# Optimization experiments

Measured on AMD Instinct MI355X. Metric: run time of the kernel, lower is better.

The kernel has to match this reference:

```python
import jax, jax.numpy as jnp
import numpy as np

N_NODES = 50000
N_EDGES = 600000
D = 128
BN_EPS = 1e-5


def _linear_init(key, fan_in, fan_out):
    # torch nn.Linear default: U(-1/sqrt(fan_in), 1/sqrt(fan_in)) for W and b
    kw, kb = jax.random.split(key)
    bound = 1.0 / np.sqrt(fan_in)
    W = jax.random.uniform(kw, (fan_in, fan_out), minval=-bound, maxval=bound, dtype=jnp.float32)
    b = jax.random.uniform(kb, (fan_out,), minval=-bound, maxval=bound, dtype=jnp.float32)
    return W, b


def setup_inputs() -> dict:
    key = jax.random.key(0)
    ks = jax.random.split(key, 8)
    x = jax.random.normal(ks[0], (N_NODES, D), dtype=jnp.float32)
    edge_index = jax.random.randint(ks[1], (2, N_EDGES), 0, N_NODES, dtype=jnp.int32)
    edge_attr = jax.random.normal(ks[2], (N_EDGES, D), dtype=jnp.float32)
    # MLP: [2D, D, D, D] -> Linear(2D,D)+SiLU+BN, Linear(D,D)+SiLU+BN, Linear(D,D)
    W1, b1 = _linear_init(ks[3], 2 * D, D)
    W2, b2 = _linear_init(ks[4], D, D)
    W3, b3 = _linear_init(ks[5], D, D)
    g1 = jnp.ones((D,), jnp.float32); be1 = jnp.zeros((D,), jnp.float32)
    g2 = jnp.ones((D,), jnp.float32); be2 = jnp.zeros((D,), jnp.float32)
    return {"x": x, "edge_index": edge_index, "edge_attr": edge_attr,
            "W1": W1, "b1": b1, "g1": g1, "be1": be1,
            "W2": W2, "b2": b2, "g2": g2, "be2": be2,
            "W3": W3, "b3": b3}


def _bn(h, gamma, beta):
    # BatchNorm1d in training mode: normalize with batch statistics (biased var)
    mean = jnp.mean(h, axis=0)
    var = jnp.var(h, axis=0)
    return (h - mean) * jax.lax.rsqrt(var + BN_EPS) * gamma + beta


def reference(x, edge_index, edge_attr, W1, b1, g1, be1, W2, b2, g2, be2, W3, b3):
    src = edge_index[0]
    # scatter_add over edges indexed by source node -> [N_NODES, D]
    agg = jax.ops.segment_sum(edge_attr, src, num_segments=x.shape[0])
    h = jnp.concatenate([x, agg], axis=1)  # [N, 2D]
    h = _bn(jax.nn.silu(h @ W1 + b1), g1, be1)
    h = _bn(jax.nn.silu(h @ W2 + b2), g2, be2)
    return h @ W3 + b3
```

## Files before the change

kernel.cpp:

```cpp
#include <hip/hip_runtime.h>
#include <hip/hip_bf16.h>

#define D 128

typedef __attribute__((ext_vector_type(8))) short bfrag;
typedef __attribute__((ext_vector_type(4))) float facc;
typedef __attribute__((ext_vector_type(4))) unsigned int u32x4;
typedef __attribute__((ext_vector_type(4))) float f32x4;

__device__ __forceinline__ facc mfma16(bfrag a, bfrag b, facc c) {
    return __builtin_amdgcn_mfma_f32_16x16x32_bf16(a, b, c, 0, 0, 0);
}
__device__ __forceinline__ unsigned int bf16_rn(float f) {
    unsigned int u = __float_as_uint(f);
    u += 0x7FFF + ((u >> 16) & 1);
    return u >> 16;
}
__device__ __forceinline__ float bf16_f(unsigned int h) {
    return __uint_as_float(h << 16);
}
__device__ __forceinline__ unsigned int packf(float v) {
    unsigned int hi = bf16_rn(v);
    unsigned int lo = bf16_rn(v - bf16_f(hi));
    return (hi << 16) | lo;
}

__global__ __launch_bounds__(256) void prep_kernel(
    const int* __restrict__ src, int* __restrict__ counts, int nedges,
    const float* __restrict__ x, unsigned int* __restrict__ xp, int n4,
    const float* __restrict__ W1, unsigned short* __restrict__ Wh,
    unsigned short* __restrict__ Wl, int eblk, int sblk) {
    int b = blockIdx.x;
    if (b < eblk) {
        int e = b * 256 + threadIdx.x;
        if (e < nedges) atomicAdd(&counts[src[e]], 1);
    } else if (b < eblk + sblk) {
        int i = (b - eblk) * 256 + threadIdx.x;
        if (i < n4) {
            float4 v = ((const float4*)x)[i];
            uint4 p;
            p.x = packf(v.x);
            p.y = packf(v.y);
            p.z = packf(v.z);
            p.w = packf(v.w);
            ((uint4*)xp)[i] = p;
        }
    } else {
        int j = b - eblk - sblk;
        int k = threadIdx.x;
        float w = W1[(size_t)k * D + j];
        unsigned int hi = bf16_rn(w);
        size_t o = (size_t)((k >> 3) * 128 + j) * 8 + (k & 7);
        Wh[o] = (unsigned short)hi;
        Wl[o] = (unsigned short)bf16_rn(w - bf16_f(hi));
    }
}

#define SCHUNK 2048
__global__ __launch_bounds__(256) void scan1_kernel(
    const int* __restrict__ counts, int* __restrict__ bsum, int n) {
    __shared__ int sd[256];
    const int tid = threadIdx.x;
    const int base = blockIdx.x * SCHUNK + tid * 8;
    int s = 0;
#pragma unroll
    for (int j = 0; j < 8; ++j) {
        int idx = base + j;
        if (idx < n) s += counts[idx];
    }
    sd[tid] = s;
    __syncthreads();
    for (int d2 = 128; d2; d2 >>= 1) {
        if (tid < d2) sd[tid] += sd[tid + d2];
        __syncthreads();
    }
    if (tid == 0) bsum[blockIdx.x] = sd[0];
}
__global__ void scan2_kernel(int* __restrict__ bsum, int nb) {
    int tid = threadIdx.x;
    int v = (tid < nb) ? bsum[tid] : 0;
#pragma unroll
    for (int d2 = 1; d2 < 64; d2 <<= 1) {
        int t = __shfl_up(v, d2);
        if (tid >= d2) v += t;
    }
    if (tid < nb) bsum[tid] = v;
}
__global__ __launch_bounds__(256) void scan3_kernel(
    const int* __restrict__ counts, const int* __restrict__ bsum,
    int* __restrict__ off, int* __restrict__ cur, int n) {
    __shared__ int sd[256];
    const int tid = threadIdx.x;
    const int base = blockIdx.x * SCHUNK + tid * 8;
    int loc[8];
    int s = 0;
#pragma unroll
    for (int j = 0; j < 8; ++j) {
        int idx = base + j;
        int c = (idx < n) ? counts[idx] : 0;
        loc[j] = c;
        s += c;
    }
    sd[tid] = s;
    __syncthreads();
#pragma unroll
    for (int d2 = 1; d2 < 256; d2 <<= 1) {
        int t = (tid >= d2) ? sd[tid - d2] : 0;
        __syncthreads();
        sd[tid] += t;
        __syncthreads();
    }
    int boff = (blockIdx.x == 0) ? 0 : bsum[blockIdx.x - 1];
    int pre = boff + sd[tid] - s;
#pragma unroll
    for (int j = 0; j < 8; ++j) {
        int idx = base + j;
        if (idx < n) {
            off[idx] = pre;
            cur[idx] = pre;
            pre += loc[j];
        }
    }
    if (tid == 255 && base + 8 >= n && n <= blockIdx.x * SCHUNK + SCHUNK)
        off[n] = boff + sd[255];
}

__global__ void fill_kernel(const int* __restrict__ src, int* __restrict__ cur,
                            int* __restrict__ eid, int nedges) {
    int e = blockIdx.x * 256 + threadIdx.x;
    if (e < nedges) {
        int slot = atomicAdd(&cur[src[e]], 1);
        eid[slot] = e;
    }
}

__global__ __launch_bounds__(256) void gather_kernel(
    const float* __restrict__ edge_attr, const int* __restrict__ eid,
    const int* __restrict__ off, unsigned int* __restrict__ aggp, int nnodes) {
    int node = blockIdx.x * 4 + (threadIdx.x >> 6);
    int lane = threadIdx.x & 63;
    if (node >= nnodes) return;
    const int h = lane >> 5;
    const int c = lane & 31;
    int i = off[node];
    const int e = off[node + 1];
    f32x4 acc = {0.f, 0.f, 0.f, 0.f};

    if (i < e && (i & 1)) {
        f32x4 v = __builtin_nontemporal_load(
            (const f32x4*)(edge_attr + (size_t)eid[i] * D) + c);
        if (h == 0) acc += v;
        ++i;
    }
    for (; i + 16 <= e; i += 16) {
        f32x4 v[8];
#pragma unroll
        for (int u = 0; u < 8; ++u) {
            int2 ep = *(const int2*)(eid + i + 2 * u);
            int row = h ? ep.y : ep.x;
            v[u] = __builtin_nontemporal_load(
                (const f32x4*)(edge_attr + (size_t)row * D) + c);
        }
#pragma unroll
        for (int u = 0; u < 8; ++u) acc += v[u];
    }
    for (; i + 2 <= e; i += 2) {
        int2 ep = *(const int2*)(eid + i);
        int row = h ? ep.y : ep.x;
        acc += __builtin_nontemporal_load(
            (const f32x4*)(edge_attr + (size_t)row * D) + c);
    }
    if (i < e) {
        f32x4 v = __builtin_nontemporal_load(
            (const f32x4*)(edge_attr + (size_t)eid[i] * D) + c);
        if (h == 0) acc += v;
    }
#pragma unroll
    for (int r = 0; r < 4; ++r) acc[r] += __shfl_xor(acc[r], 32);
    if (h == 0) {
        u32x4 p;
#pragma unroll
        for (int r = 0; r < 4; ++r) p[r] = packf(acc[r]);
        *((u32x4*)(aggp + (size_t)node * D) + c) = p;
    }
}

__global__ void fold_kernel(const float* __restrict__ sum,
                            const float* __restrict__ sq,
                            const float* __restrict__ gamma,
                            const float* __restrict__ beta,
                            const float* __restrict__ W,
                            const float* __restrict__ b,
                            unsigned short* __restrict__ Wh,
                            unsigned short* __restrict__ Wl,
                            float* __restrict__ bf, float invM) {
    int j = blockIdx.x;
    int k = threadIdx.x;
    float mean = sum[k] * invM;
    float var = sq[k] * invM - mean * mean;
    float scale = gamma[k] * rsqrtf(var + 1e-5f);
    float shift = beta[k] - mean * scale;
    float w = W[k * D + j];
    float wf = scale * w;
    unsigned int hi = bf16_rn(wf);
    size_t o = (size_t)((k >> 3) * 128 + j) * 8 + (k & 7);
    Wh[o] = (unsigned short)hi;
    Wl[o] = (unsigned short)bf16_rn(wf - bf16_f(hi));
    float v = shift * w;
#pragma unroll
    for (int of = 32; of; of >>= 1) v += __shfl_down(v, of);
    __shared__ float ws2[2];
    if ((k & 63) == 0) ws2[k >> 6] = v;
    __syncthreads();
    if (k == 0) bf[j] = b[j] + ws2[0] + ws2[1];
}

template <int K, bool SILU, bool STATS, bool PACKOUT>
__global__ __launch_bounds__(256, 2) void gemm_mfma(
    const unsigned int* __restrict__ A0, const unsigned int* __restrict__ A1,
    const unsigned short* __restrict__ Wh,
    const unsigned short* __restrict__ Wl,
    const float* __restrict__ bias, unsigned int* __restrict__ Cp,
    float* __restrict__ Cf, float* __restrict__ gsum,
    float* __restrict__ gsq, int M) {
    constexpr int NS = K / 32;
    const int tid = threadIdx.x;
    const int w = tid >> 6;
    const int l = tid & 63;
    const int lr = l & 15;
    const int lk = l >> 4;
    const int row0 = blockIdx.x * 128 + w * 32;

    facc acc[2][8];
#pragma unroll
    for (int rt = 0; rt < 2; ++rt)
#pragma unroll
        for (int ct = 0; ct < 8; ++ct)
#pragma unroll
            for (int r = 0; r < 4; ++r) acc[rt][ct][r] = 0.f;

    for (int s = 0; s < NS; ++s) {
        const int kb = s * 32 + lk * 8;
        bfrag ah[2], al[2];
#pragma unroll
        for (int rt = 0; rt < 2; ++rt) {
            const int arow = row0 + rt * 16 + lr;
            const unsigned int* As = A0;
            int kk = kb;
            if (K == 256 && s >= 4) { As = A1; kk = kb - 128; }
            u32x4 q0 = {0u, 0u, 0u, 0u}, q1 = {0u, 0u, 0u, 0u};
            if (arow < M) {
                const u32x4* p = (const u32x4*)(As + (size_t)arow * D + kk);
                q0 = p[0];
                q1 = p[1];
            }
            unsigned int ua[8] = {q0.x, q0.y, q0.z, q0.w,
                                  q1.x, q1.y, q1.z, q1.w};
            u32x4 uh, ul;
#pragma unroll
            for (int r = 0; r < 4; ++r) {
                uh[r] = __builtin_amdgcn_perm(ua[2 * r + 1], ua[2 * r],
                                              0x07060302u);
                ul[r] = __builtin_amdgcn_perm(ua[2 * r + 1], ua[2 * r],
                                              0x05040100u);
            }
            ah[rt] = __builtin_bit_cast(bfrag, uh);
            al[rt] = __builtin_bit_cast(bfrag, ul);
        }
        bfrag bh[8], bl[8];
        const int fb = (s * 4 + lk) * 128;
#pragma unroll
        for (int ct = 0; ct < 8; ++ct) {
            size_t o = (size_t)(fb + ct * 16 + lr) * 8;
            bh[ct] = *(const bfrag*)(Wh + o);
            bl[ct] = *(const bfrag*)(Wl + o);
        }
#pragma unroll
        for (int rt = 0; rt < 2; ++rt)
#pragma unroll
            for (int ct = 0; ct < 8; ++ct)
                acc[rt][ct] = mfma16(ah[rt], bh[ct], acc[rt][ct]);
#pragma unroll
        for (int rt = 0; rt < 2; ++rt)
#pragma unroll
            for (int ct = 0; ct < 8; ++ct)
                acc[rt][ct] = mfma16(ah[rt], bl[ct], acc[rt][ct]);
#pragma unroll
        for (int rt = 0; rt < 2; ++rt)
#pragma unroll
            for (int ct = 0; ct < 8; ++ct)
                acc[rt][ct] = mfma16(al[rt], bh[ct], acc[rt][ct]);
    }

    __shared__ float sred[2][4][128];
#pragma unroll
    for (int ct = 0; ct < 8; ++ct) {
        const int col = ct * 16 + lr;
        const float bj = bias[col];
        float s = 0.f, q = 0.f;
#pragma unroll
        for (int rt = 0; rt < 2; ++rt) {
            const int base = row0 + rt * 16 + lk * 4;
#pragma unroll
            for (int r = 0; r < 4; ++r) {
                int crow = base + r;
                if (crow < M) {
                    float v = acc[rt][ct][r] + bj;
                    if (SILU) v = v / (1.0f + __expf(-v));
                    if (PACKOUT) Cp[(size_t)crow * D + col] = packf(v);
                    else         Cf[(size_t)crow * D + col] = v;
                    if (STATS) { s += v; q += v * v; }
                }
            }
        }
        if (STATS) {
            s += __shfl_xor(s, 16);
            s += __shfl_xor(s, 32);
            q += __shfl_xor(q, 16);
            q += __shfl_xor(q, 32);
            if (lk == 0) {
                sred[0][w][col] = s;
                sred[1][w][col] = q;
            }
        }
    }
    if (STATS) {
        __syncthreads();
        if (tid < 128) {
            float v = sred[0][0][tid] + sred[0][1][tid] + sred[0][2][tid] +
                      sred[0][3][tid];
            unsafeAtomicAdd(&gsum[tid], v);
        } else {
            int c = tid - 128;
            float v = sred[1][0][c] + sred[1][1][c] + sred[1][2][c] +
                      sred[1][3][c];
            unsafeAtomicAdd(&gsq[c], v);
        }
    }
}

extern "C" void kernel_launch(void* const* d_in, const int* in_sizes, int n_in,
                              void* d_out, int out_size, void* d_ws,
                              size_t ws_size, hipStream_t stream) {
    const float* x     = (const float*)d_in[0];
    const int*   eidx  = (const int*)d_in[1];
    const float* eattr = (const float*)d_in[2];
    const float* W1  = (const float*)d_in[3];
    const float* b1  = (const float*)d_in[4];
    const float* g1  = (const float*)d_in[5];
    const float* be1 = (const float*)d_in[6];
    const float* W2  = (const float*)d_in[7];
    const float* b2  = (const float*)d_in[8];
    const float* g2  = (const float*)d_in[9];
    const float* be2 = (const float*)d_in[10];
    const float* W3  = (const float*)d_in[11];
    const float* b3  = (const float*)d_in[12];

    const int M = in_sizes[0] / D;
    const int E = in_sizes[1] / 2;
    const int* srcIdx = eidx;

    unsigned int* wsu = (unsigned int*)d_ws;
    unsigned int* aggp = wsu;
    unsigned int* xp   = aggp + (size_t)M * D;
    unsigned int* h1p  = xp + (size_t)M * D;
    unsigned int* h2p  = h1p + (size_t)M * D;
    float* sum1 = (float*)(h2p + (size_t)M * D);
    float* sq1  = sum1 + D;
    float* sum2 = sq1 + D;
    float* sq2  = sum2 + D;
    float* b2f  = sq2 + D;
    float* b3f  = b2f + D;
    int* counts = (int*)(b3f + D);
    int* off    = counts + M;
    int* cur    = off + M + 4;
    int* eid    = cur + M;
    int* bsum   = eid + E;
    unsigned short* W1h = (unsigned short*)(bsum + 64);
    unsigned short* W1l = W1h + 256 * D;
    unsigned short* W2h = W1l + 256 * D;
    unsigned short* W2l = W2h + D * D;
    unsigned short* W3h = W2l + D * D;
    unsigned short* W3l = W3h + D * D;

    float* out = (float*)d_out;

    hipMemsetAsync(counts, 0, (size_t)M * sizeof(int), stream);
    hipMemsetAsync(sum1, 0, 4 * D * sizeof(float), stream);

    const int eblk = (E + 255) / 256;
    const int sblk = (M * 32 + 255) / 256;
    prep_kernel<<<eblk + sblk + 128, 256, 0, stream>>>(
        srcIdx, counts, E, x, xp, M * 32, W1, W1h, W1l, eblk, sblk);

    const int nb = (M + SCHUNK - 1) / SCHUNK;
    scan1_kernel<<<nb, 256, 0, stream>>>(counts, bsum, M);
    scan2_kernel<<<1, 64, 0, stream>>>(bsum, nb);
    scan3_kernel<<<nb, 256, 0, stream>>>(counts, bsum, off, cur, M);
    fill_kernel<<<eblk, 256, 0, stream>>>(srcIdx, cur, eid, E);
    gather_kernel<<<(M + 3) / 4, 256, 0, stream>>>(eattr, eid, off, aggp, M);

    int nblk = (M + 127) / 128;
    gemm_mfma<256, true, true, true><<<nblk, 256, 0, stream>>>(
        xp, aggp, W1h, W1l, b1, h1p, nullptr, sum1, sq1, M);
    fold_kernel<<<D, D, 0, stream>>>(sum1, sq1, g1, be1, W2, b2, W2h, W2l,
                                     b2f, 1.0f / (float)M);
    gemm_mfma<128, true, true, true><<<nblk, 256, 0, stream>>>(
        h1p, nullptr, W2h, W2l, b2f, h2p, nullptr, sum2, sq2, M);
    fold_kernel<<<D, D, 0, stream>>>(sum2, sq2, g2, be2, W3, b3, W3h, W3l,
                                     b3f, 1.0f / (float)M);
    gemm_mfma<128, false, false, false><<<nblk, 256, 0, stream>>>(
        h2p, nullptr, W3h, W3l, b3f, nullptr, out, nullptr, nullptr, M);
}
```

Measured before the change: 247.7 us.

## Scatter bf16 edge rows into CSR order and fuse aggregation into first GEMM

Instead of building an edge-id permutation and gathering fp32 edge rows at random, the fill pass now reads each edge row once, converts it to bf16 and writes it into its CSR slot. The first GEMM then sums the contiguous, sorted rows per node into shared memory and consumes them directly as the second half of K. This removes the separate gather kernel, the eid indirection and the aggregated fp32 round trip. It trades a bf16 rounding of edge attributes, which lowers accuracy of the sums, and a 64-row tile GEMM with serial per-node aggregation.

```diff
diff --git a/kernel.cpp b/kernel.cpp
--- a/kernel.cpp
+++ b/kernel.cpp
@@ -6,6 +6,7 @@
 typedef __attribute__((ext_vector_type(8))) short bfrag;
 typedef __attribute__((ext_vector_type(4))) float facc;
 typedef __attribute__((ext_vector_type(4))) unsigned int u32x4;
+typedef __attribute__((ext_vector_type(2))) unsigned int u32x2;
 typedef __attribute__((ext_vector_type(4))) float f32x4;
 
 __device__ __forceinline__ facc mfma16(bfrag a, bfrag b, facc c) {
@@ -23,6 +24,12 @@
     unsigned int hi = bf16_rn(v);
     unsigned int lo = bf16_rn(v - bf16_f(hi));
     return (hi << 16) | lo;
+}
+__device__ __forceinline__ float bf16lo(unsigned int u) {
+    return __uint_as_float(u << 16);
+}
+__device__ __forceinline__ float bf16hi(unsigned int u) {
+    return __uint_as_float(u & 0xFFFF0000u);
 }
 
 __global__ __launch_bounds__(256) void prep_kernel(
@@ -125,63 +132,185 @@
         off[n] = boff + sd[255];
 }
 
-__global__ void fill_kernel(const int* __restrict__ src, int* __restrict__ cur,
-                            int* __restrict__ eid, int nedges) {
-    int e = blockIdx.x * 256 + threadIdx.x;
-    if (e < nedges) {
-        int slot = atomicAdd(&cur[src[e]], 1);
-        eid[slot] = e;
-    }
-}
-
-__global__ __launch_bounds__(256) void gather_kernel(
-    const float* __restrict__ edge_attr, const int* __restrict__ eid,
-    const int* __restrict__ off, unsigned int* __restrict__ aggp, int nnodes) {
-    int node = blockIdx.x * 4 + (threadIdx.x >> 6);
-    int lane = threadIdx.x & 63;
-    if (node >= nnodes) return;
-    const int h = lane >> 5;
-    const int c = lane & 31;
-    int i = off[node];
-    const int e = off[node + 1];
-    f32x4 acc = {0.f, 0.f, 0.f, 0.f};
-
-    if (i < e && (i & 1)) {
-        f32x4 v = __builtin_nontemporal_load(
-            (const f32x4*)(edge_attr + (size_t)eid[i] * D) + c);
-        if (h == 0) acc += v;
-        ++i;
-    }
-    for (; i + 16 <= e; i += 16) {
-        f32x4 v[8];
-#pragma unroll
-        for (int u = 0; u < 8; ++u) {
-            int2 ep = *(const int2*)(eid + i + 2 * u);
-            int row = h ? ep.y : ep.x;
-            v[u] = __builtin_nontemporal_load(
-                (const f32x4*)(edge_attr + (size_t)row * D) + c);
-        }
-#pragma unroll
-        for (int u = 0; u < 8; ++u) acc += v[u];
-    }
-    for (; i + 2 <= e; i += 2) {
-        int2 ep = *(const int2*)(eid + i);
-        int row = h ? ep.y : ep.x;
-        acc += __builtin_nontemporal_load(
-            (const f32x4*)(edge_attr + (size_t)row * D) + c);
-    }
-    if (i < e) {
-        f32x4 v = __builtin_nontemporal_load(
-            (const f32x4*)(edge_attr + (size_t)eid[i] * D) + c);
-        if (h == 0) acc += v;
-    }
-#pragma unroll
-    for (int r = 0; r < 4; ++r) acc[r] += __shfl_xor(acc[r], 32);
-    if (h == 0) {
-        u32x4 p;
-#pragma unroll
-        for (int r = 0; r < 4; ++r) p[r] = packf(acc[r]);
-        *((u32x4*)(aggp + (size_t)node * D) + c) = p;
+__global__ __launch_bounds__(256) void fillp_kernel(
+    const float* __restrict__ edge_attr, const int* __restrict__ src,
+    int* __restrict__ cur, unsigned int* __restrict__ ebS, int nedges) {
+    const int l = threadIdx.x & 63;
+    const int h = l >> 5;
+    const int c = l & 31;
+    int e = blockIdx.x * 8 + (threadIdx.x >> 6) * 2 + h;
+    if (e >= nedges) return;
+    f32x4 v = __builtin_nontemporal_load(
+        (const f32x4*)(edge_attr + (size_t)e * D) + c);
+    int slot = 0;
+    if (c == 0) slot = atomicAdd(&cur[src[e]], 1);
+    slot = __shfl(slot, l & 32);
+    u32x2 p;
+    p.x = bf16_rn(v[0]) | (bf16_rn(v[1]) << 16);
+    p.y = bf16_rn(v[2]) | (bf16_rn(v[3]) << 16);
+    *((u32x2*)(ebS + (size_t)slot * 64) + c) = p;
+}
+
+__global__ __launch_bounds__(256, 2) void gemm1_fused(
+    const unsigned int* __restrict__ xp, const unsigned int* __restrict__ ebS,
+    const int* __restrict__ off, const unsigned short* __restrict__ Wh,
+    const unsigned short* __restrict__ Wl, const float* __restrict__ bias,
+    unsigned int* __restrict__ h1p, float* __restrict__ gsum,
+    float* __restrict__ gsq, int M) {
+    __shared__ unsigned int As[64][132];
+    __shared__ float sred[2][4][128];
+    const int tid = threadIdx.x;
+    const int w = tid >> 6;
+    const int l = tid & 63;
+    const int h = l >> 5;
+    const int c = l & 31;
+    const int row0 = blockIdx.x * 64;
+
+    for (int nd = 0; nd < 16; ++nd) {
+        int node = row0 + w * 16 + nd;
+        if (node >= M) break;
+        int s = off[node];
+        const int e = off[node + 1];
+        f32x4 acc = {0.f, 0.f, 0.f, 0.f};
+        int i = s;
+        for (; i + 16 <= e; i += 16) {
+            u32x2 q[8];
+#pragma unroll
+            for (int u = 0; u < 8; ++u)
+                q[u] = __builtin_nontemporal_load(
+                    (const u32x2*)(ebS + (size_t)(i + 2 * u + h) * 64) + c);
+#pragma unroll
+            for (int u = 0; u < 8; ++u) {
+                acc[0] += bf16lo(q[u].x);
+                acc[1] += bf16hi(q[u].x);
+                acc[2] += bf16lo(q[u].y);
+                acc[3] += bf16hi(q[u].y);
+            }
+        }
+        for (; i + 2 <= e; i += 2) {
+            u32x2 q = __builtin_nontemporal_load(
+                (const u32x2*)(ebS + (size_t)(i + h) * 64) + c);
+            acc[0] += bf16lo(q.x);
+            acc[1] += bf16hi(q.x);
+            acc[2] += bf16lo(q.y);
+            acc[3] += bf16hi(q.y);
+        }
+        if (i < e && h == 0) {
+            u32x2 q = __builtin_nontemporal_load(
+                (const u32x2*)(ebS + (size_t)i * 64) + c);
+            acc[0] += bf16lo(q.x);
+            acc[1] += bf16hi(q.x);
+            acc[2] += bf16lo(q.y);
+            acc[3] += bf16hi(q.y);
+        }
+#pragma unroll
+        for (int r = 0; r < 4; ++r) acc[r] += __shfl_xor(acc[r], 32);
+        if (h == 0) {
+            u32x4 p;
+#pragma unroll
+            for (int r = 0; r < 4; ++r) p[r] = packf(acc[r]);
+            *(u32x4*)&As[w * 16 + nd][c * 4] = p;
+        }
+    }
+    __syncthreads();
+
+    const int lr = l & 15;
+    const int lk = l >> 4;
+    facc acc[8];
+#pragma unroll
+    for (int ct = 0; ct < 8; ++ct)
+#pragma unroll
+        for (int r = 0; r < 4; ++r) acc[ct][r] = 0.f;
+
+    for (int s = 0; s < 8; ++s) {
+        unsigned int ua[8];
+        if (s < 4) {
+            const int arow = row0 + w * 16 + lr;
+            const int kk = s * 32 + lk * 8;
+            u32x4 q0 = {0u, 0u, 0u, 0u}, q1 = {0u, 0u, 0u, 0u};
+            if (arow < M) {
+                const u32x4* p = (const u32x4*)(xp + (size_t)arow * D + kk);
+                q0 = p[0];
+                q1 = p[1];
+            }
+#pragma unroll
+            for (int r = 0; r < 4; ++r) {
+                ua[r] = q0[r];
+                ua[4 + r] = q1[r];
+            }
+        } else {
+            const int kk = (s - 4) * 32 + lk * 8;
+            const u32x4* p = (const u32x4*)&As[w * 16 + lr][kk];
+            u32x4 q0 = p[0], q1 = p[1];
+#pragma unroll
+            for (int r = 0; r < 4; ++r) {
+                ua[r] = q0[r];
+                ua[4 + r] = q1[r];
+            }
+        }
+        u32x4 uh, ul;
+#pragma unroll
+        for (int r = 0; r < 4; ++r) {
+            uh[r] = __builtin_amdgcn_perm(ua[2 * r + 1], ua[2 * r],
+                                          0x07060302u);
+            ul[r] = __builtin_amdgcn_perm(ua[2 * r + 1], ua[2 * r],
+                                          0x05040100u);
+        }
+        bfrag ah = __builtin_bit_cast(bfrag, uh);
+        bfrag al = __builtin_bit_cast(bfrag, ul);
+
+        bfrag bh[8], bl[8];
+        const int fb = (s * 4 + lk) * 128;
+#pragma unroll
+        for (int ct = 0; ct < 8; ++ct) {
+            size_t o = (size_t)(fb + ct * 16 + lr) * 8;
+            bh[ct] = *(const bfrag*)(Wh + o);
+            bl[ct] = *(const bfrag*)(Wl + o);
+        }
+#pragma unroll
+        for (int ct = 0; ct < 8; ++ct) acc[ct] = mfma16(ah, bh[ct], acc[ct]);
+#pragma unroll
+        for (int ct = 0; ct < 8; ++ct) acc[ct] = mfma16(ah, bl[ct], acc[ct]);
+#pragma unroll
+        for (int ct = 0; ct < 8; ++ct) acc[ct] = mfma16(al, bh[ct], acc[ct]);
+    }
+
+#pragma unroll
+    for (int ct = 0; ct < 8; ++ct) {
+        const int col = ct * 16 + lr;
+        const float bj = bias[col];
+        float s = 0.f, q = 0.f;
+        const int base = row0 + w * 16 + lk * 4;
+#pragma unroll
+        for (int r = 0; r < 4; ++r) {
+            int crow = base + r;
+            if (crow < M) {
+                float v = acc[ct][r] + bj;
+                v = v / (1.0f + __expf(-v));
+                h1p[(size_t)crow * D + col] = packf(v);
+                s += v;
+                q += v * v;
+            }
+        }
+        s += __shfl_xor(s, 16);
+        s += __shfl_xor(s, 32);
+        q += __shfl_xor(q, 16);
+        q += __shfl_xor(q, 32);
+        if (lk == 0) {
+            sred[0][w][col] = s;
+            sred[1][w][col] = q;
+        }
+    }
+    __syncthreads();
+    if (tid < 128) {
+        float v = sred[0][0][tid] + sred[0][1][tid] + sred[0][2][tid] +
+                  sred[0][3][tid];
+        unsafeAtomicAdd(&gsum[tid], v);
+    } else {
+        int cc = tid - 128;
+        float v = sred[1][0][cc] + sred[1][1][cc] + sred[1][2][cc] +
+                  sred[1][3][cc];
+        unsafeAtomicAdd(&gsq[cc], v);
     }
 }
 
@@ -215,15 +344,14 @@
     if (k == 0) bf[j] = b[j] + ws2[0] + ws2[1];
 }
 
-template <int K, bool SILU, bool STATS, bool PACKOUT>
+template <bool SILU, bool STATS, bool PACKOUT>
 __global__ __launch_bounds__(256, 2) void gemm_mfma(
-    const unsigned int* __restrict__ A0, const unsigned int* __restrict__ A1,
+    const unsigned int* __restrict__ A0,
     const unsigned short* __restrict__ Wh,
     const unsigned short* __restrict__ Wl,
     const float* __restrict__ bias, unsigned int* __restrict__ Cp,
     float* __restrict__ Cf, float* __restrict__ gsum,
     float* __restrict__ gsq, int M) {
-    constexpr int NS = K / 32;
     const int tid = threadIdx.x;
     const int w = tid >> 6;
     const int l = tid & 63;
@@ -239,18 +367,15 @@
 #pragma unroll
             for (int r = 0; r < 4; ++r) acc[rt][ct][r] = 0.f;
 
-    for (int s = 0; s < NS; ++s) {
+    for (int s = 0; s < 4; ++s) {
         const int kb = s * 32 + lk * 8;
         bfrag ah[2], al[2];
 #pragma unroll
         for (int rt = 0; rt < 2; ++rt) {
             const int arow = row0 + rt * 16 + lr;
-            const unsigned int* As = A0;
-            int kk = kb;
-            if (K == 256 && s >= 4) { As = A1; kk = kb - 128; }
             u32x4 q0 = {0u, 0u, 0u, 0u}, q1 = {0u, 0u, 0u, 0u};
             if (arow < M) {
-                const u32x4* p = (const u32x4*)(As + (size_t)arow * D + kk);
+                const u32x4* p = (const u32x4*)(A0 + (size_t)arow * D + kb);
                 q0 = p[0];
                 q1 = p[1];
             }
@@ -361,10 +486,10 @@
     const int* srcIdx = eidx;
 
     unsigned int* wsu = (unsigned int*)d_ws;
-    unsigned int* aggp = wsu;
-    unsigned int* xp   = aggp + (size_t)M * D;
-    unsigned int* h1p  = xp + (size_t)M * D;
-    unsigned int* h2p  = h1p + (size_t)M * D;
+    unsigned int* ebS = wsu;
+    unsigned int* xp  = ebS + (size_t)E * 64;
+    unsigned int* h1p = xp + (size_t)M * D;
+    unsigned int* h2p = h1p + (size_t)M * D;
     float* sum1 = (float*)(h2p + (size_t)M * D);
     float* sq1  = sum1 + D;
     float* sum2 = sq1 + D;
@@ -374,8 +499,7 @@
     int* counts = (int*)(b3f + D);
     int* off    = counts + M;
     int* cur    = off + M + 4;
-    int* eid    = cur + M;
-    int* bsum   = eid + E;
+    int* bsum   = cur + M;
     unsigned short* W1h = (unsigned short*)(bsum + 64);
     unsigned short* W1l = W1h + 256 * D;
     unsigned short* W2h = W1l + 256 * D;
@@ -385,8 +509,8 @@
 
     float* out = (float*)d_out;
 
-    hipMemsetAsync(counts, 0, (size_t)M * sizeof(int), stream);
-    hipMemsetAsync(sum1, 0, 4 * D * sizeof(float), stream);
+    (void)hipMemsetAsync(counts, 0, (size_t)M * sizeof(int), stream);
+    (void)hipMemsetAsync(sum1, 0, 4 * D * sizeof(float), stream);
 
     const int eblk = (E + 255) / 256;
     const int sblk = (M * 32 + 255) / 256;
@@ -397,18 +521,19 @@
     scan1_kernel<<<nb, 256, 0, stream>>>(counts, bsum, M);
     scan2_kernel<<<1, 64, 0, stream>>>(bsum, nb);
     scan3_kernel<<<nb, 256, 0, stream>>>(counts, bsum, off, cur, M);
-    fill_kernel<<<eblk, 256, 0, stream>>>(srcIdx, cur, eid, E);
-    gather_kernel<<<(M + 3) / 4, 256, 0, stream>>>(eattr, eid, off, aggp, M);
+
+    fillp_kernel<<<(E + 7) / 8, 256, 0, stream>>>(eattr, srcIdx, cur, ebS, E);
+
+    gemm1_fused<<<(M + 63) / 64, 256, 0, stream>>>(
+        xp, ebS, off, W1h, W1l, b1, h1p, sum1, sq1, M);
 
     int nblk = (M + 127) / 128;
-    gemm_mfma<256, true, true, true><<<nblk, 256, 0, stream>>>(
-        xp, aggp, W1h, W1l, b1, h1p, nullptr, sum1, sq1, M);
     fold_kernel<<<D, D, 0, stream>>>(sum1, sq1, g1, be1, W2, b2, W2h, W2l,
                                      b2f, 1.0f / (float)M);
-    gemm_mfma<128, true, true, true><<<nblk, 256, 0, stream>>>(
-        h1p, nullptr, W2h, W2l, b2f, h2p, nullptr, sum2, sq2, M);
+    gemm_mfma<true, true, true><<<nblk, 256, 0, stream>>>(
+        h1p, W2h, W2l, b2f, h2p, nullptr, sum2, sq2, M);
     fold_kernel<<<D, D, 0, stream>>>(sum2, sq2, g2, be2, W3, b3, W3h, W3l,
                                      b3f, 1.0f / (float)M);
-    gemm_mfma<128, false, false, false><<<nblk, 256, 0, stream>>>(
-        h2p, nullptr, W3h, W3l, b3f, nullptr, out, nullptr, nullptr, M);
-}
+    gemm_mfma<false, false, false><<<nblk, 256, 0, stream>>>(
+        h2p, W3h, W3l, b3f, nullptr, out, nullptr, nullptr, M);
+}
```

Result: slower. 279.6 us (+12.9%).

## Scatter edge attributes into source-sorted bf16 buffer, then gather contiguously

Applied to the files above, without the earlier changes.

The fill pass now reads each edge_attr row once, converts it to bf16, and writes it to its sorted slot in a packed buffer. The gather then sums contiguous bf16 rows per node instead of doing random fp32 reads through an edge-id indirection. The aim is to cut gather bandwidth and remove the random indirect access. The cost is an extra full write plus read of the edge data and a loss of precision, since the aggregated inputs are rounded to single bf16 rather than kept in fp32 (the old path packed hi/lo).

```diff
diff --git a/kernel.cpp b/kernel.cpp
--- a/kernel.cpp
+++ b/kernel.cpp
@@ -6,6 +6,7 @@
 typedef __attribute__((ext_vector_type(8))) short bfrag;
 typedef __attribute__((ext_vector_type(4))) float facc;
 typedef __attribute__((ext_vector_type(4))) unsigned int u32x4;
+typedef __attribute__((ext_vector_type(2))) unsigned int u32x2;
 typedef __attribute__((ext_vector_type(4))) float f32x4;
 
 __device__ __forceinline__ facc mfma16(bfrag a, bfrag b, facc c) {
@@ -23,6 +24,12 @@
     unsigned int hi = bf16_rn(v);
     unsigned int lo = bf16_rn(v - bf16_f(hi));
     return (hi << 16) | lo;
+}
+__device__ __forceinline__ float bf16lo(unsigned int u) {
+    return __uint_as_float(u << 16);
+}
+__device__ __forceinline__ float bf16hi(unsigned int u) {
+    return __uint_as_float(u & 0xFFFF0000u);
 }
 
 __global__ __launch_bounds__(256) void prep_kernel(
@@ -125,18 +132,32 @@
         off[n] = boff + sd[255];
 }
 
-__global__ void fill_kernel(const int* __restrict__ src, int* __restrict__ cur,
-                            int* __restrict__ eid, int nedges) {
-    int e = blockIdx.x * 256 + threadIdx.x;
-    if (e < nedges) {
-        int slot = atomicAdd(&cur[src[e]], 1);
-        eid[slot] = e;
-    }
-}
-
-__global__ __launch_bounds__(256) void gather_kernel(
-    const float* __restrict__ edge_attr, const int* __restrict__ eid,
-    const int* __restrict__ off, unsigned int* __restrict__ aggp, int nnodes) {
+__global__ __launch_bounds__(256) void fillp_kernel(
+    const float* __restrict__ edge_attr, const int* __restrict__ src,
+    int* __restrict__ cur, unsigned int* __restrict__ ebS, int nedges) {
+    const int l = threadIdx.x & 63;
+    const int h = l >> 5;
+    const int c = l & 31;
+    const int e0 = blockIdx.x * 16 + (threadIdx.x >> 6) * 2 + h;
+#pragma unroll
+    for (int rep = 0; rep < 2; ++rep) {
+        int e = e0 + rep * 8;
+        if (e >= nedges) continue;
+        f32x4 v = __builtin_nontemporal_load(
+            (const f32x4*)(edge_attr + (size_t)e * D) + c);
+        int slot = 0;
+        if (c == 0) slot = atomicAdd(&cur[src[e]], 1);
+        slot = __shfl(slot, l & 32);
+        u32x2 p;
+        p.x = bf16_rn(v[0]) | (bf16_rn(v[1]) << 16);
+        p.y = bf16_rn(v[2]) | (bf16_rn(v[3]) << 16);
+        *((u32x2*)(ebS + (size_t)slot * 64) + c) = p;
+    }
+}
+
+__global__ __launch_bounds__(256) void gatherS_kernel(
+    const unsigned int* __restrict__ ebS, const int* __restrict__ off,
+    unsigned int* __restrict__ aggp, int nnodes) {
     int node = blockIdx.x * 4 + (threadIdx.x >> 6);
     int lane = threadIdx.x & 63;
     if (node >= nnodes) return;
@@ -145,35 +166,35 @@
     int i = off[node];
     const int e = off[node + 1];
     f32x4 acc = {0.f, 0.f, 0.f, 0.f};
-
-    if (i < e && (i & 1)) {
-        f32x4 v = __builtin_nontemporal_load(
-            (const f32x4*)(edge_attr + (size_t)eid[i] * D) + c);
-        if (h == 0) acc += v;
-        ++i;
-    }
-    for (; i + 16 <= e; i += 16) {
-        f32x4 v[8];
-#pragma unroll
-        for (int u = 0; u < 8; ++u) {
-            int2 ep = *(const int2*)(eid + i + 2 * u);
-            int row = h ? ep.y : ep.x;
-            v[u] = __builtin_nontemporal_load(
-                (const f32x4*)(edge_attr + (size_t)row * D) + c);
-        }
-#pragma unroll
-        for (int u = 0; u < 8; ++u) acc += v[u];
+    for (; i + 8 <= e; i += 8) {
+        u32x2 q[4];
+#pragma unroll
+        for (int u = 0; u < 4; ++u)
+            q[u] = __builtin_nontemporal_load(
+                (const u32x2*)(ebS + (size_t)(i + 2 * u + h) * 64) + c);
+#pragma unroll
+        for (int u = 0; u < 4; ++u) {
+            acc[0] += bf16lo(q[u].x);
+            acc[1] += bf16hi(q[u].x);
+            acc[2] += bf16lo(q[u].y);
+            acc[3] += bf16hi(q[u].y);
+        }
     }
     for (; i + 2 <= e; i += 2) {
-        int2 ep = *(const int2*)(eid + i);
-        int row = h ? ep.y : ep.x;
-        acc += __builtin_nontemporal_load(
-            (const f32x4*)(edge_attr + (size_t)row * D) + c);
-    }
-    if (i < e) {
-        f32x4 v = __builtin_nontemporal_load(
-            (const f32x4*)(edge_attr + (size_t)eid[i] * D) + c);
-        if (h == 0) acc += v;
+        u32x2 q = __builtin_nontemporal_load(
+            (const u32x2*)(ebS + (size_t)(i + h) * 64) + c);
+        acc[0] += bf16lo(q.x);
+        acc[1] += bf16hi(q.x);
+        acc[2] += bf16lo(q.y);
+        acc[3] += bf16hi(q.y);
+    }
+    if (i < e && h == 0) {
+        u32x2 q = __builtin_nontemporal_load(
+            (const u32x2*)(ebS + (size_t)i * 64) + c);
+        acc[0] += bf16lo(q.x);
+        acc[1] += bf16hi(q.x);
+        acc[2] += bf16lo(q.y);
+        acc[3] += bf16hi(q.y);
     }
 #pragma unroll
     for (int r = 0; r < 4; ++r) acc[r] += __shfl_xor(acc[r], 32);
@@ -361,10 +382,10 @@
     const int* srcIdx = eidx;
 
     unsigned int* wsu = (unsigned int*)d_ws;
-    unsigned int* aggp = wsu;
-    unsigned int* xp   = aggp + (size_t)M * D;
-    unsigned int* h1p  = xp + (size_t)M * D;
-    unsigned int* h2p  = h1p + (size_t)M * D;
+    unsigned int* ebS = wsu;
+    unsigned int* xp  = ebS + (size_t)E * 64;
+    unsigned int* h1p = xp + (size_t)M * D;
+    unsigned int* h2p = h1p + (size_t)M * D;
     float* sum1 = (float*)(h2p + (size_t)M * D);
     float* sq1  = sum1 + D;
     float* sum2 = sq1 + D;
@@ -374,8 +395,7 @@
     int* counts = (int*)(b3f + D);
     int* off    = counts + M;
     int* cur    = off + M + 4;
-    int* eid    = cur + M;
-    int* bsum   = eid + E;
+    int* bsum   = cur + M;
     unsigned short* W1h = (unsigned short*)(bsum + 64);
     unsigned short* W1l = W1h + 256 * D;
     unsigned short* W2h = W1l + 256 * D;
@@ -383,10 +403,12 @@
     unsigned short* W3h = W2l + D * D;
     unsigned short* W3l = W3h + D * D;
 
+    unsigned int* aggp = h2p;
+
     float* out = (float*)d_out;
 
-    hipMemsetAsync(counts, 0, (size_t)M * sizeof(int), stream);
-    hipMemsetAsync(sum1, 0, 4 * D * sizeof(float), stream);
+    (void)hipMemsetAsync(counts, 0, (size_t)M * sizeof(int), stream);
+    (void)hipMemsetAsync(sum1, 0, 4 * D * sizeof(float), stream);
 
     const int eblk = (E + 255) / 256;
     const int sblk = (M * 32 + 255) / 256;
@@ -397,8 +419,10 @@
     scan1_kernel<<<nb, 256, 0, stream>>>(counts, bsum, M);
     scan2_kernel<<<1, 64, 0, stream>>>(bsum, nb);
     scan3_kernel<<<nb, 256, 0, stream>>>(counts, bsum, off, cur, M);
-    fill_kernel<<<eblk, 256, 0, stream>>>(srcIdx, cur, eid, E);
-    gather_kernel<<<(M + 3) / 4, 256, 0, stream>>>(eattr, eid, off, aggp, M);
+
+    fillp_kernel<<<(E + 15) / 16, 256, 0, stream>>>(eattr, srcIdx, cur, ebS, E);
+
+    gatherS_kernel<<<(M + 3) / 4, 256, 0, stream>>>(ebS, off, aggp, M);
 
     int nblk = (M + 127) / 128;
     gemm_mfma<256, true, true, true><<<nblk, 256, 0, stream>>>(
```

New measurement: 258.2 us. 4.2% more time.
